# Kernel tuning notes

Hardware: AMD Instinct MI355X
Metric: run time of the kernel (lower is better)

The kernel has to match this reference:

```python
import jax, jax.numpy as jnp
import numpy as np

N_ENT, E, M, STEPS, B, H, C = 500000, 128, 8, 3, 4096, 256, 16

def setup_inputs() -> dict:
    key = jax.random.key(0)
    ks = jax.random.split(key, 13)
    s = 0.05
    return {
        "entity_ids": jax.random.randint(ks[0], (B, STEPS + 1), 0, N_ENT),
        "module_ids": jax.random.randint(ks[1], (B, STEPS), 0, M),
        "embedding": jax.random.normal(ks[2], (N_ENT, E), jnp.float32),
        "W_in": jax.random.normal(ks[3], (M, E, E), jnp.float32) * s,
        "b_in": jax.random.normal(ks[4], (M, E), jnp.float32) * s,
        "W_bias": jax.random.normal(ks[5], (M, E, E), jnp.float32) * s,
        "b_bias": jax.random.normal(ks[6], (M, E), jnp.float32) * s,
        "W_f": jax.random.normal(ks[7], (M, 2 * E, E), jnp.float32) * s,
        "b_f": jax.random.normal(ks[8], (M, E), jnp.float32) * s,
        "W1": jax.random.normal(ks[9], (E, H), jnp.float32) * s,
        "b1": jax.random.normal(ks[10], (H,), jnp.float32) * s,
        "W2": jax.random.normal(ks[11], (H, C), jnp.float32) * s,
        "b2": jax.random.normal(ks[12], (C,), jnp.float32) * s,
    }

def reference(entity_ids, module_ids, embedding, W_in, b_in, W_bias, b_bias,
              W_f, b_f, W1, b1, W2, b2):
    # x: [B, E] embedding of each path's start entity
    x = embedding[entity_ids[:, 0]]

    def step(x, inputs):
        mid, eid = inputs                      # [B], [B]
        bias = embedding[eid]                  # [B, E]
        h_in = jax.nn.relu(jnp.einsum('be,beo->bo', x, W_in[mid]) + b_in[mid])
        h_bi = jax.nn.relu(jnp.einsum('be,beo->bo', bias, W_bias[mid]) + b_bias[mid])
        h = jnp.concatenate([h_in, h_bi], axis=1)  # [B, 2E]
        x_new = jnp.tanh(jnp.einsum('bf,bfo->bo', h, W_f[mid]) + b_f[mid])
        return x_new, None

    xs = (module_ids.T, entity_ids[:, 1:].T)   # [STEPS, B] each
    x, _ = jax.lax.scan(step, x, xs)

    # classifier: Linear -> ReLU -> Linear
    h = jax.nn.relu(x @ W1 + b1)
    return h @ W2 + b2
```

## Files before the change

### kernel.cpp

```cpp
#include <hip/hip_runtime.h>

#define BB      4096
#define EE      128
#define MM      8
#define NSTEPS  3
#define HH      256
#define CC      16

#define TS      16
#define NBMAX   (BB/TS + MM)
#define FB      1024

#define NFRAGBLK 1096

#define ECONV0   1096
#define COUNT0   2120
#define GRID1    2168

typedef __attribute__((ext_vector_type(8))) short  bf16x8;
typedef __attribute__((ext_vector_type(4))) float  f32x4;

__device__ __forceinline__ unsigned short bf16_rn(float v) {
    unsigned u = __float_as_uint(v);
    return (unsigned short)((u + 0x7FFFu + ((u >> 16) & 1u)) >> 16);
}
__device__ __forceinline__ float bf16_f(unsigned short h) {
    return __uint_as_float(((unsigned)h) << 16);
}
__device__ __forceinline__ void split8(const float* v, bf16x8& hi, bf16x8& lo) {
    #pragma unroll
    for (int i = 0; i < 8; i++) {
        unsigned short h = bf16_rn(v[i]);
        hi[i] = (short)h;
        lo[i] = (short)bf16_rn(v[i] - bf16_f(h));
    }
}
__device__ __forceinline__ void split1(float v, unsigned short& h, unsigned short& l) {
    h = bf16_rn(v);
    l = bf16_rn(v - bf16_f(h));
}
#define MFMA(a,b,c) __builtin_amdgcn_mfma_f32_16x16x32_bf16((a),(b),(c),0,0,0)
__device__ __forceinline__ f32x4 mfma3(bf16x8 ah, bf16x8 al, bf16x8 bh, bf16x8 bl, f32x4 c) {
    c = MFMA(ah, bh, c);
    c = MFMA(ah, bl, c);
    c = MFMA(al, bh, c);
    return c;
}

__global__ __launch_bounds__(256) void convert_kernel(
    const int*   __restrict__ entity_ids, const int* __restrict__ module_ids,
    const float* __restrict__ embedding,
    const float* __restrict__ W_in, const float* __restrict__ W_bias,
    const float* __restrict__ W_f,  const float* __restrict__ W1,
    const float* __restrict__ W2,
    unsigned short* __restrict__ wf,
    unsigned short* __restrict__ x0h, unsigned short* __restrict__ x0l,
    unsigned short* __restrict__ ebh, unsigned short* __restrict__ ebl,
    int* __restrict__ wcnt)
{
    const int b = blockIdx.x, tid = threadIdx.x;
    if (b < NFRAGBLK) {
        unsigned short* dhi = wf + (size_t)b * FB;
        unsigned short* dlo = dhi + 512;
        #pragma unroll
        for (int half = 0; half < 2; half++) {
            const int el = tid + half * 256;
            const int ln = el >> 3, j = el & 7;
            const int krel = ((ln >> 4) << 3) + j;
            const int nrel = ln & 15;
            float v;
            if (b < 512) {
                const int bb = b & 255;
                const int kc = bb & 3, nt = (bb >> 2) & 7, m = bb >> 5;
                const float* src = (b < 256 ? W_in : W_bias) + (size_t)m * EE * EE;
                v = src[(size_t)(kc*32 + krel) * EE + nt*16 + nrel];
            } else if (b < 1024) {
                const int bb = b - 512;
                const int kc = bb & 7, nt = (bb >> 3) & 7, m = bb >> 6;
                v = W_f[(size_t)m * 2*EE*EE + (size_t)(kc*32 + krel) * EE + nt*16 + nrel];
            } else if (b < 1088) {
                const int bb = b - 1024;
                const int kc = bb & 3, nt = bb >> 2;
                v = W1[(size_t)(kc*32 + krel) * HH + nt*16 + nrel];
            } else {
                const int kc = b - 1088;
                v = W2[(size_t)(kc*32 + krel) * CC + nrel];
            }
            split1(v, dhi[el], dlo[el]);
        }
    } else if (b < COUNT0) {
        const int u = b - ECONV0;
        const int g = u >> 8, wb = u & 255;
        const int rloc = tid >> 4, cpart = tid & 15;
        const int s = wb*16 + rloc;
        const int eid = entity_ids[s*(NSTEPS+1) + g];
        const float* src = embedding + (size_t)eid*EE + cpart*8;
        float vv[8];
        *(float4*)(vv)     = *(const float4*)(src);
        *(float4*)(vv + 4) = *(const float4*)(src + 4);
        bf16x8 hi, lo;
        split8(vv, hi, lo);
        unsigned short* dh = (g == 0 ? x0h : ebh + (size_t)(g-1)*BB*EE) + (size_t)s*EE + cpart*8;
        unsigned short* dl = (g == 0 ? x0l : ebl + (size_t)(g-1)*BB*EE) + (size_t)s*EE + cpart*8;
        *(bf16x8*)dh = hi;
        *(bf16x8*)dl = lo;
    } else {
        const int u = b - COUNT0;
        const int t = u >> 4, chunk = u & 15;
        const int wave = tid >> 6, lane = tid & 63;
        const int s = chunk*256 + wave*64 + lane;
        const int m = module_ids[s*NSTEPS + t];
        unsigned long long bal[MM];
        #pragma unroll
        for (int k = 0; k < MM; k++) bal[k] = __ballot(m == k);
        if (lane < MM)
            wcnt[((t*16 + chunk)*4 + wave)*MM + lane] = __popcll(bal[lane]);
    }
}

__global__ __launch_bounds__(256) void plan_kernel(
    const int* __restrict__ wcnt,
    int* __restrict__ blockMod,
    int* __restrict__ gbase,
    int* __restrict__ perm)
{
    __shared__ int scnt[NSTEPS*16*4*MM];
    __shared__ int tot [NSTEPS][MM];
    __shared__ int base[NSTEPS][MM];
    const int tid = threadIdx.x;

    for (int i = tid; i < NSTEPS*16*4*MM; i += 256) scnt[i] = wcnt[i];
    for (int i = tid; i < NSTEPS*NBMAX*TS; i += 256) perm[i] = -1;
    __syncthreads();

    if (tid < NSTEPS*MM) {
        const int t = tid / MM, m = tid % MM;
        int s = 0;
        for (int sl = 0; sl < 64; sl++) s += scnt[(t*64 + sl)*MM + m];
        tot[t][m] = s;
    }
    __syncthreads();
    if (tid < NSTEPS) {
        const int t = tid;
        int blk = 0;
        for (int m = 0; m < MM; m++) {
            base[t][m] = blk * TS;
            const int nb = (tot[t][m] + TS - 1) / TS;
            for (int b = 0; b < nb; b++) blockMod[t*NBMAX + blk + b] = m;
            blk += nb;
        }
        for (; blk < NBMAX; blk++) blockMod[t*NBMAX + blk] = -1;
    }
    __syncthreads();
    if (tid < NSTEPS*MM) {
        const int t = tid / MM, m = tid % MM;
        int run = base[t][m];
        for (int sl = 0; sl < 64; sl++) {
            const int idx = (t*64 + sl)*MM + m;
            gbase[idx] = run;
            run += scnt[idx];
        }
    }
}

__global__ __launch_bounds__(256) void scatter_kernel(
    const int* __restrict__ module_ids,
    const int* __restrict__ gbase,
    int* __restrict__ perm)
{
    const int u = blockIdx.x;
    const int t = u >> 4, chunk = u & 15;
    const int tid = threadIdx.x, wave = tid >> 6, lane = tid & 63;
    __shared__ int gb[4*MM];
    if (tid < 4*MM) gb[tid] = gbase[((t*16 + chunk)*4)*MM + tid];
    __syncthreads();

    const int s = chunk*256 + wave*64 + lane;
    const int m = module_ids[s*NSTEPS + t];
    unsigned long long bal[MM];
    #pragma unroll
    for (int k = 0; k < MM; k++) bal[k] = __ballot(m == k);
    const unsigned long long below = (1ull << lane) - 1ull;
    const int rank = __popcll(bal[m] & below);
    perm[t*NBMAX*TS + gb[wave*MM + m] + rank] = s;
}

__global__ __launch_bounds__(512) void step_kernel(
    const int t,
    const unsigned short* __restrict__ x0h, const unsigned short* __restrict__ x0l,
    const unsigned short* __restrict__ ebh, const unsigned short* __restrict__ ebl,
    const float* __restrict__ b_in, const float* __restrict__ b_bias,
    const float* __restrict__ b_f,
    const unsigned short* __restrict__ wf,
    const int*   __restrict__ blockMod,
    const int*   __restrict__ perm,
    unsigned short* __restrict__ xsh, unsigned short* __restrict__ xsl)
{
    const int bid = blockIdx.x;
    const int m = blockMod[t*NBMAX + bid];
    if (m < 0) return;
    const int tid  = threadIdx.x;
    const int lane = tid & 63, wave = tid >> 6;
    const int row16 = lane & 15, quad = lane >> 4;
    const int pb = (t*NBMAX + bid)*TS;

    __shared__ __align__(16) unsigned short hfh[8][512];
    __shared__ __align__(16) unsigned short hfl[8][512];
    __shared__ int sids[TS];

    if (tid < TS) sids[tid] = perm[pb + tid];
    __syncthreads();

    const int sA  = sids[row16];
    const int sAc = sA < 0 ? 0 : sA;

    const unsigned short* xh_p = (t == 0 ? x0h : xsh) + (size_t)sAc*EE;
    const unsigned short* xl_p = (t == 0 ? x0l : xsl) + (size_t)sAc*EE;
    const unsigned short* eh_p = ebh + (size_t)t*BB*EE + (size_t)sAc*EE;
    const unsigned short* el_p = ebl + (size_t)t*BB*EE + (size_t)sAc*EE;

    bf16x8 xh[4], xl[4], eh[4], el_[4];
    #pragma unroll
    for (int kc = 0; kc < 4; kc++) {
        const int off = kc*32 + quad*8;
        xh[kc]  = *(const bf16x8*)(xh_p + off);
        xl[kc]  = *(const bf16x8*)(xl_p + off);
        eh[kc]  = *(const bf16x8*)(eh_p + off);
        el_[kc] = *(const bf16x8*)(el_p + off);
    }

    f32x4 aci = {0.f,0.f,0.f,0.f}, acb = {0.f,0.f,0.f,0.f};
    #pragma unroll
    for (int kc = 0; kc < 4; kc++) {
        const unsigned short* bI = wf + (size_t)((m*8 + wave)*4 + kc)*FB;
        const unsigned short* bB = wf + (size_t)(256 + (m*8 + wave)*4 + kc)*FB;
        const bf16x8 wih = *(const bf16x8*)(bI + lane*8);
        const bf16x8 wil = *(const bf16x8*)(bI + 512 + lane*8);
        const bf16x8 wbh = *(const bf16x8*)(bB + lane*8);
        const bf16x8 wbl = *(const bf16x8*)(bB + 512 + lane*8);
        aci = mfma3(xh[kc], xl[kc], wih, wil, aci);
        acb = mfma3(eh[kc], el_[kc], wbh, wbl, acb);
    }

    {
        const int col = wave*16 + row16;
        const float bin = b_in [m*EE + col];
        const float bbi = b_bias[m*EE + col];
        #pragma unroll
        for (int r = 0; r < 4; r++) {
            const int row = quad*4 + r;
            {
                const float v = fmaxf(aci[r] + bin, 0.f);
                const int k = col, kc = k >> 5;
                const int idx = (row + 16*((k >> 3) & 3))*8 + (k & 7);
                split1(v, hfh[kc][idx], hfl[kc][idx]);
            }
            {
                const float v = fmaxf(acb[r] + bbi, 0.f);
                const int k = EE + col, kc = k >> 5;
                const int idx = (row + 16*((k >> 3) & 3))*8 + (k & 7);
                split1(v, hfh[kc][idx], hfl[kc][idx]);
            }
        }
    }
    __syncthreads();

    f32x4 acf = {0.f,0.f,0.f,0.f};
    #pragma unroll
    for (int kc = 0; kc < 8; kc++) {
        const bf16x8 ah = *(const bf16x8*)(&hfh[kc][lane*8]);
        const bf16x8 al = *(const bf16x8*)(&hfl[kc][lane*8]);
        const unsigned short* bF = wf + (size_t)(512 + (m*8 + wave)*8 + kc)*FB;
        const bf16x8 wfh = *(const bf16x8*)(bF + lane*8);
        const bf16x8 wfl = *(const bf16x8*)(bF + 512 + lane*8);
        acf = mfma3(ah, al, wfh, wfl, acf);
    }
    {
        const int col = wave*16 + row16;
        const float bfv = b_f[m*EE + col];
        #pragma unroll
        for (int r = 0; r < 4; r++) {
            const int s = sids[quad*4 + r];
            if (s >= 0) {
                const float v = tanhf(acf[r] + bfv);
                unsigned short h, l;
                split1(v, h, l);
                xsh[(size_t)s*EE + col] = h;
                xsl[(size_t)s*EE + col] = l;
            }
        }
    }
}

__global__ __launch_bounds__(512) void final_kernel(
    const unsigned short* __restrict__ xsh, const unsigned short* __restrict__ xsl,
    const float* __restrict__ b1v, const float* __restrict__ b2,
    const unsigned short* __restrict__ wf,
    float* __restrict__ out)
{
    const int tid = threadIdx.x, bid = blockIdx.x;
    const int lane = tid & 63, wave = tid >> 6;
    const int row16 = lane & 15, quad = lane >> 4;
    const int sbase = bid * TS;

    __shared__ __align__(16) unsigned short hfh[8][512];
    __shared__ __align__(16) unsigned short hfl[8][512];
    __shared__ float red[8][TS][CC];

    const unsigned short* xh_p = xsh + (size_t)(sbase + row16)*EE;
    const unsigned short* xl_p = xsl + (size_t)(sbase + row16)*EE;
    bf16x8 xh[4], xl[4];
    #pragma unroll
    for (int kc = 0; kc < 4; kc++) {
        const int off = kc*32 + quad*8;
        xh[kc] = *(const bf16x8*)(xh_p + off);
        xl[kc] = *(const bf16x8*)(xl_p + off);
    }

    f32x4 a1[2] = {{0.f,0.f,0.f,0.f},{0.f,0.f,0.f,0.f}};
    #pragma unroll
    for (int i = 0; i < 2; i++) {
        const int nt = wave + 8*i;
        #pragma unroll
        for (int kc = 0; kc < 4; kc++) {
            const unsigned short* bW = wf + (size_t)(1024 + nt*4 + kc)*FB;
            const bf16x8 wh = *(const bf16x8*)(bW + lane*8);
            const bf16x8 wl = *(const bf16x8*)(bW + 512 + lane*8);
            a1[i] = mfma3(xh[kc], xl[kc], wh, wl, a1[i]);
        }
    }
    #pragma unroll
    for (int i = 0; i < 2; i++) {
        const int col = (wave + 8*i)*16 + row16;
        const float b = b1v[col];
        #pragma unroll
        for (int r = 0; r < 4; r++) {
            const int row = quad*4 + r;
            const float v = fmaxf(a1[i][r] + b, 0.f);
            const int kc = col >> 5;
            const int idx = (row + 16*((col >> 3) & 3))*8 + (col & 7);
            split1(v, hfh[kc][idx], hfl[kc][idx]);
        }
    }
    __syncthreads();

    f32x4 a2 = {0.f,0.f,0.f,0.f};
    {
        const int kc = wave;
        const bf16x8 ah = *(const bf16x8*)(&hfh[kc][lane*8]);
        const bf16x8 al = *(const bf16x8*)(&hfl[kc][lane*8]);
        const unsigned short* bW = wf + (size_t)(1088 + kc)*FB;
        const bf16x8 wh = *(const bf16x8*)(bW + lane*8);
        const bf16x8 wl = *(const bf16x8*)(bW + 512 + lane*8);
        a2 = mfma3(ah, al, wh, wl, a2);
    }
    #pragma unroll
    for (int r = 0; r < 4; r++) red[wave][quad*4 + r][row16] = a2[r];
    __syncthreads();

    if (tid < TS*CC) {
        const int s = tid >> 4, c = tid & 15;
        float v = b2[c];
        #pragma unroll
        for (int w = 0; w < 8; w++) v += red[w][s][c];
        out[(size_t)(sbase + s)*CC + c] = v;
    }
}

extern "C" void kernel_launch(void* const* d_in, const int* in_sizes, int n_in,
                              void* d_out, int out_size, void* d_ws, size_t ws_size,
                              hipStream_t stream) {
    const int*   entity_ids = (const int*)  d_in[0];
    const int*   module_ids = (const int*)  d_in[1];
    const float* embedding  = (const float*)d_in[2];
    const float* W_in   = (const float*)d_in[3];
    const float* b_in   = (const float*)d_in[4];
    const float* W_bias = (const float*)d_in[5];
    const float* b_bias = (const float*)d_in[6];
    const float* W_f    = (const float*)d_in[7];
    const float* b_f    = (const float*)d_in[8];
    const float* W1     = (const float*)d_in[9];
    const float* b1     = (const float*)d_in[10];
    const float* W2     = (const float*)d_in[11];
    const float* b2     = (const float*)d_in[12];
    float* out = (float*)d_out;

    char* ws = (char*)d_ws;
    int* blockMod = (int*)(ws + 0);
    int* perm     = (int*)(ws + 4096);
    int* wcnt     = (int*)(ws + 54784);
    int* gbase    = (int*)(ws + 60928);
    unsigned short* wfb = (unsigned short*)(ws + 131072);
    unsigned short* x0h = (unsigned short*)(ws + (4u<<20));
    unsigned short* x0l = (unsigned short*)(ws + (5u<<20));
    unsigned short* xsh = (unsigned short*)(ws + (6u<<20));
    unsigned short* xsl = (unsigned short*)(ws + (7u<<20));
    unsigned short* ebh = (unsigned short*)(ws + (8u<<20));
    unsigned short* ebl = (unsigned short*)(ws + (11u<<20));

    convert_kernel<<<GRID1, 256, 0, stream>>>(entity_ids, module_ids, embedding,
                                              W_in, W_bias, W_f, W1, W2,
                                              wfb, x0h, x0l, ebh, ebl, wcnt);
    plan_kernel<<<1, 256, 0, stream>>>(wcnt, blockMod, gbase, perm);
    scatter_kernel<<<48, 256, 0, stream>>>(module_ids, gbase, perm);
    for (int t = 0; t < NSTEPS; t++) {
        step_kernel<<<NBMAX, 512, 0, stream>>>(t, x0h, x0l, ebh, ebl,
                                               b_in, b_bias, b_f,
                                               wfb, blockMod, perm, xsh, xsl);
    }
    final_kernel<<<BB/TS, 512, 0, stream>>>(xsh, xsl, b1, b2, wfb, out);
}
```

Before: 370.1 us.

## Fuse all stages into one cooperative persistent kernel with grid syncs

Merges the convert, plan, scatter, three step kernels and the classifier into a single persistent mega kernel of 256 blocks. The kernel steps through phases separated by grid-wide cooperative syncs, and falls back to six separate launches if the cooperative launch fails. Module bucketing switches from a count/plan/scatter pipeline to per-wave ballots with atomicAdd into per-(step,module) counters, which removes the single-block plan kernel. The aim is to cut launch overhead and serial tiny kernels. In exchange, work is grid-strided over fewer blocks and every phase boundary costs a grid sync.

```diff
diff --git a/kernel.cpp b/kernel.cpp
--- a/kernel.cpp
+++ b/kernel.cpp
@@ -1,4 +1,7 @@
 #include <hip/hip_runtime.h>
+#include <hip/hip_cooperative_groups.h>
+
+namespace cg = cooperative_groups;
 
 #define BB      4096
 #define EE      128
@@ -8,14 +11,13 @@
 #define CC      16
 
 #define TS      16
-#define NBMAX   (BB/TS + MM)
 #define FB      1024
 
 #define NFRAGBLK 1096
 
-#define ECONV0   1096
-#define COUNT0   2120
-#define GRID1    2168
+#define CAP     4096
+#define GRIDN   256
+#define NV0     (NFRAGBLK + 512)
 
 typedef __attribute__((ext_vector_type(8))) short  bf16x8;
 typedef __attribute__((ext_vector_type(4))) float  f32x4;
@@ -47,323 +49,274 @@
     return c;
 }
 
-__global__ __launch_bounds__(256) void convert_kernel(
+__global__ __launch_bounds__(512, 2) void mega_kernel(
+    int ph_lo, int ph_hi, int coop,
     const int*   __restrict__ entity_ids, const int* __restrict__ module_ids,
     const float* __restrict__ embedding,
-    const float* __restrict__ W_in, const float* __restrict__ W_bias,
-    const float* __restrict__ W_f,  const float* __restrict__ W1,
-    const float* __restrict__ W2,
+    const float* __restrict__ W_in,  const float* __restrict__ b_in,
+    const float* __restrict__ W_bias,const float* __restrict__ b_bias,
+    const float* __restrict__ W_f,   const float* __restrict__ b_f,
+    const float* __restrict__ W1,    const float* __restrict__ b1v,
+    const float* __restrict__ W2,    const float* __restrict__ b2,
+    float* __restrict__ out,
+    int* __restrict__ cnt, int* __restrict__ perm,
     unsigned short* __restrict__ wf,
     unsigned short* __restrict__ x0h, unsigned short* __restrict__ x0l,
-    unsigned short* __restrict__ ebh, unsigned short* __restrict__ ebl,
-    int* __restrict__ wcnt)
+    unsigned short* __restrict__ xsh, unsigned short* __restrict__ xsl,
+    unsigned short* __restrict__ ebh, unsigned short* __restrict__ ebl)
 {
-    const int b = blockIdx.x, tid = threadIdx.x;
-    if (b < NFRAGBLK) {
-        unsigned short* dhi = wf + (size_t)b * FB;
-        unsigned short* dlo = dhi + 512;
-        #pragma unroll
-        for (int half = 0; half < 2; half++) {
-            const int el = tid + half * 256;
-            const int ln = el >> 3, j = el & 7;
-            const int krel = ((ln >> 4) << 3) + j;
-            const int nrel = ln & 15;
-            float v;
-            if (b < 512) {
-                const int bb = b & 255;
-                const int kc = bb & 3, nt = (bb >> 2) & 7, m = bb >> 5;
-                const float* src = (b < 256 ? W_in : W_bias) + (size_t)m * EE * EE;
-                v = src[(size_t)(kc*32 + krel) * EE + nt*16 + nrel];
-            } else if (b < 1024) {
-                const int bb = b - 512;
-                const int kc = bb & 7, nt = (bb >> 3) & 7, m = bb >> 6;
-                v = W_f[(size_t)m * 2*EE*EE + (size_t)(kc*32 + krel) * EE + nt*16 + nrel];
-            } else if (b < 1088) {
-                const int bb = b - 1024;
-                const int kc = bb & 3, nt = bb >> 2;
-                v = W1[(size_t)(kc*32 + krel) * HH + nt*16 + nrel];
-            } else {
-                const int kc = b - 1088;
-                v = W2[(size_t)(kc*32 + krel) * CC + nrel];
-            }
-            split1(v, dhi[el], dlo[el]);
-        }
-    } else if (b < COUNT0) {
-        const int u = b - ECONV0;
-        const int g = u >> 8, wb = u & 255;
-        const int rloc = tid >> 4, cpart = tid & 15;
-        const int s = wb*16 + rloc;
-        const int eid = entity_ids[s*(NSTEPS+1) + g];
-        const float* src = embedding + (size_t)eid*EE + cpart*8;
-        float vv[8];
-        *(float4*)(vv)     = *(const float4*)(src);
-        *(float4*)(vv + 4) = *(const float4*)(src + 4);
-        bf16x8 hi, lo;
-        split8(vv, hi, lo);
-        unsigned short* dh = (g == 0 ? x0h : ebh + (size_t)(g-1)*BB*EE) + (size_t)s*EE + cpart*8;
-        unsigned short* dl = (g == 0 ? x0l : ebl + (size_t)(g-1)*BB*EE) + (size_t)s*EE + cpart*8;
-        *(bf16x8*)dh = hi;
-        *(bf16x8*)dl = lo;
-    } else {
-        const int u = b - COUNT0;
-        const int t = u >> 4, chunk = u & 15;
-        const int wave = tid >> 6, lane = tid & 63;
-        const int s = chunk*256 + wave*64 + lane;
-        const int m = module_ids[s*NSTEPS + t];
-        unsigned long long bal[MM];
-        #pragma unroll
-        for (int k = 0; k < MM; k++) bal[k] = __ballot(m == k);
-        if (lane < MM)
-            wcnt[((t*16 + chunk)*4 + wave)*MM + lane] = __popcll(bal[lane]);
-    }
-}
-
-__global__ __launch_bounds__(256) void plan_kernel(
-    const int* __restrict__ wcnt,
-    int* __restrict__ blockMod,
-    int* __restrict__ gbase,
-    int* __restrict__ perm)
-{
-    __shared__ int scnt[NSTEPS*16*4*MM];
-    __shared__ int tot [NSTEPS][MM];
-    __shared__ int base[NSTEPS][MM];
-    const int tid = threadIdx.x;
-
-    for (int i = tid; i < NSTEPS*16*4*MM; i += 256) scnt[i] = wcnt[i];
-    for (int i = tid; i < NSTEPS*NBMAX*TS; i += 256) perm[i] = -1;
-    __syncthreads();
-
-    if (tid < NSTEPS*MM) {
-        const int t = tid / MM, m = tid % MM;
-        int s = 0;
-        for (int sl = 0; sl < 64; sl++) s += scnt[(t*64 + sl)*MM + m];
-        tot[t][m] = s;
-    }
-    __syncthreads();
-    if (tid < NSTEPS) {
-        const int t = tid;
-        int blk = 0;
-        for (int m = 0; m < MM; m++) {
-            base[t][m] = blk * TS;
-            const int nb = (tot[t][m] + TS - 1) / TS;
-            for (int b = 0; b < nb; b++) blockMod[t*NBMAX + blk + b] = m;
-            blk += nb;
-        }
-        for (; blk < NBMAX; blk++) blockMod[t*NBMAX + blk] = -1;
-    }
-    __syncthreads();
-    if (tid < NSTEPS*MM) {
-        const int t = tid / MM, m = tid % MM;
-        int run = base[t][m];
-        for (int sl = 0; sl < 64; sl++) {
-            const int idx = (t*64 + sl)*MM + m;
-            gbase[idx] = run;
-            run += scnt[idx];
-        }
-    }
-}
-
-__global__ __launch_bounds__(256) void scatter_kernel(
-    const int* __restrict__ module_ids,
-    const int* __restrict__ gbase,
-    int* __restrict__ perm)
-{
-    const int u = blockIdx.x;
-    const int t = u >> 4, chunk = u & 15;
-    const int tid = threadIdx.x, wave = tid >> 6, lane = tid & 63;
-    __shared__ int gb[4*MM];
-    if (tid < 4*MM) gb[tid] = gbase[((t*16 + chunk)*4)*MM + tid];
-    __syncthreads();
-
-    const int s = chunk*256 + wave*64 + lane;
-    const int m = module_ids[s*NSTEPS + t];
-    unsigned long long bal[MM];
-    #pragma unroll
-    for (int k = 0; k < MM; k++) bal[k] = __ballot(m == k);
-    const unsigned long long below = (1ull << lane) - 1ull;
-    const int rank = __popcll(bal[m] & below);
-    perm[t*NBMAX*TS + gb[wave*MM + m] + rank] = s;
-}
-
-__global__ __launch_bounds__(512) void step_kernel(
-    const int t,
-    const unsigned short* __restrict__ x0h, const unsigned short* __restrict__ x0l,
-    const unsigned short* __restrict__ ebh, const unsigned short* __restrict__ ebl,
-    const float* __restrict__ b_in, const float* __restrict__ b_bias,
-    const float* __restrict__ b_f,
-    const unsigned short* __restrict__ wf,
-    const int*   __restrict__ blockMod,
-    const int*   __restrict__ perm,
-    unsigned short* __restrict__ xsh, unsigned short* __restrict__ xsl)
-{
-    const int bid = blockIdx.x;
-    const int m = blockMod[t*NBMAX + bid];
-    if (m < 0) return;
     const int tid  = threadIdx.x;
+    const int bx   = blockIdx.x, gsz = gridDim.x;
     const int lane = tid & 63, wave = tid >> 6;
     const int row16 = lane & 15, quad = lane >> 4;
-    const int pb = (t*NBMAX + bid)*TS;
 
     __shared__ __align__(16) unsigned short hfh[8][512];
     __shared__ __align__(16) unsigned short hfl[8][512];
-    __shared__ int sids[TS];
-
-    if (tid < TS) sids[tid] = perm[pb + tid];
-    __syncthreads();
-
-    const int sA  = sids[row16];
-    const int sAc = sA < 0 ? 0 : sA;
-
-    const unsigned short* xh_p = (t == 0 ? x0h : xsh) + (size_t)sAc*EE;
-    const unsigned short* xl_p = (t == 0 ? x0l : xsl) + (size_t)sAc*EE;
-    const unsigned short* eh_p = ebh + (size_t)t*BB*EE + (size_t)sAc*EE;
-    const unsigned short* el_p = ebl + (size_t)t*BB*EE + (size_t)sAc*EE;
-
-    bf16x8 xh[4], xl[4], eh[4], el_[4];
-    #pragma unroll
-    for (int kc = 0; kc < 4; kc++) {
-        const int off = kc*32 + quad*8;
-        xh[kc]  = *(const bf16x8*)(xh_p + off);
-        xl[kc]  = *(const bf16x8*)(xl_p + off);
-        eh[kc]  = *(const bf16x8*)(eh_p + off);
-        el_[kc] = *(const bf16x8*)(el_p + off);
-    }
-
-    f32x4 aci = {0.f,0.f,0.f,0.f}, acb = {0.f,0.f,0.f,0.f};
-    #pragma unroll
-    for (int kc = 0; kc < 4; kc++) {
-        const unsigned short* bI = wf + (size_t)((m*8 + wave)*4 + kc)*FB;
-        const unsigned short* bB = wf + (size_t)(256 + (m*8 + wave)*4 + kc)*FB;
-        const bf16x8 wih = *(const bf16x8*)(bI + lane*8);
-        const bf16x8 wil = *(const bf16x8*)(bI + 512 + lane*8);
-        const bf16x8 wbh = *(const bf16x8*)(bB + lane*8);
-        const bf16x8 wbl = *(const bf16x8*)(bB + 512 + lane*8);
-        aci = mfma3(xh[kc], xl[kc], wih, wil, aci);
-        acb = mfma3(eh[kc], el_[kc], wbh, wbl, acb);
-    }
-
-    {
-        const int col = wave*16 + row16;
-        const float bin = b_in [m*EE + col];
-        const float bbi = b_bias[m*EE + col];
-        #pragma unroll
-        for (int r = 0; r < 4; r++) {
-            const int row = quad*4 + r;
-            {
-                const float v = fmaxf(aci[r] + bin, 0.f);
-                const int k = col, kc = k >> 5;
-                const int idx = (row + 16*((k >> 3) & 3))*8 + (k & 7);
-                split1(v, hfh[kc][idx], hfl[kc][idx]);
+    __shared__ int   sids[TS];
+    __shared__ float red[8][TS][CC];
+
+    cg::grid_group gg = cg::this_grid();
+
+    for (int ph = ph_lo; ph <= ph_hi; ph++) {
+        if (ph == 0) {
+            if (bx == 0 && tid < NSTEPS*MM) cnt[tid] = 0;
+            for (int vb = bx; vb < NV0; vb += gsz) {
+                if (vb < NFRAGBLK) {
+                    unsigned short* dhi = wf + (size_t)vb * FB;
+                    unsigned short* dlo = dhi + 512;
+                    const int el = tid;
+                    const int ln = el >> 3, j = el & 7;
+                    const int krel = ((ln >> 4) << 3) + j;
+                    const int nrel = ln & 15;
+                    float v;
+                    if (vb < 512) {
+                        const int bb = vb & 255;
+                        const int kc = bb & 3, nt = (bb >> 2) & 7, m = bb >> 5;
+                        const float* src = (vb < 256 ? W_in : W_bias) + (size_t)m * EE * EE;
+                        v = src[(size_t)(kc*32 + krel) * EE + nt*16 + nrel];
+                    } else if (vb < 1024) {
+                        const int bb = vb - 512;
+                        const int kc = bb & 7, nt = (bb >> 3) & 7, m = bb >> 6;
+                        v = W_f[(size_t)m * 2*EE*EE + (size_t)(kc*32 + krel) * EE + nt*16 + nrel];
+                    } else if (vb < 1088) {
+                        const int bb = vb - 1024;
+                        const int kc = bb & 3, nt = bb >> 2;
+                        v = W1[(size_t)(kc*32 + krel) * HH + nt*16 + nrel];
+                    } else {
+                        const int kc = vb - 1088;
+                        v = W2[(size_t)(kc*32 + krel) * CC + nrel];
+                    }
+                    split1(v, dhi[el], dlo[el]);
+                } else {
+                    const int u = vb - NFRAGBLK;
+                    const int rloc = tid >> 4, cpart = tid & 15;
+                    const int rglob = u*32 + rloc;
+                    const int g = rglob >> 12;
+                    const int s = rglob & (BB-1);
+                    const int eid = entity_ids[s*(NSTEPS+1) + g];
+                    const float* src = embedding + (size_t)eid*EE + cpart*8;
+                    float vv[8];
+                    *(float4*)(vv)     = *(const float4*)(src);
+                    *(float4*)(vv + 4) = *(const float4*)(src + 4);
+                    bf16x8 hi, lo;
+                    split8(vv, hi, lo);
+                    unsigned short* dh = (g == 0 ? x0h : ebh + (size_t)(g-1)*BB*EE) + (size_t)s*EE + cpart*8;
+                    unsigned short* dl = (g == 0 ? x0l : ebl + (size_t)(g-1)*BB*EE) + (size_t)s*EE + cpart*8;
+                    *(bf16x8*)dh = hi;
+                    *(bf16x8*)dl = lo;
+                }
             }
-            {
-                const float v = fmaxf(acb[r] + bbi, 0.f);
-                const int k = EE + col, kc = k >> 5;
-                const int idx = (row + 16*((k >> 3) & 3))*8 + (k & 7);
-                split1(v, hfh[kc][idx], hfl[kc][idx]);
+        } else if (ph == 1) {
+            for (int vb = bx; vb < (NSTEPS*BB)/512; vb += gsz) {
+                const int gid = vb*512 + tid;
+                const int t = gid >> 12, s = gid & (BB-1);
+                const int m = module_ids[s*NSTEPS + t];
+                unsigned long long mybal = 0ull, lanebal = 0ull;
+                #pragma unroll
+                for (int k = 0; k < MM; k++) {
+                    const unsigned long long bk = __ballot(m == k);
+                    if (m == k)    mybal   = bk;
+                    if (lane == k) lanebal = bk;
+                }
+                int base = 0;
+                if (lane < MM) base = atomicAdd(&cnt[t*MM + lane], __popcll(lanebal));
+                const int mybase = __shfl(base, m);
+                const unsigned long long below = (1ull << lane) - 1ull;
+                const int rank = __popcll(mybal & below);
+                perm[((t*MM + m) << 12) + mybase + rank] = s;
+            }
+        } else if (ph <= 4) {
+            const int t = ph - 2;
+            int creg[8];
+            #pragma unroll
+            for (int k = 0; k < MM; k++) creg[k] = cnt[t*MM + k];
+            int NB = 0;
+            #pragma unroll
+            for (int k = 0; k < MM; k++) NB += (creg[k] + TS - 1) >> 4;
+
+            for (int vb = bx; vb < NB; vb += gsz) {
+                int m = -1, pref = 0, cm = 0, acc = 0;
+                #pragma unroll
+                for (int k = 0; k < MM; k++) {
+                    const int nbk = (creg[k] + TS - 1) >> 4;
+                    if (m < 0 && vb < acc + nbk) { m = k; pref = acc; cm = creg[k]; }
+                    acc += nbk;
+                }
+                const int chunk = vb - pref;
+
+                __syncthreads();
+                if (tid < TS) {
+                    const int sl = chunk*TS + tid;
+                    sids[tid] = (sl < cm) ? perm[((t*MM + m) << 12) + sl] : -1;
+                }
+                __syncthreads();
+
+                const int sA  = sids[row16];
+                const int sAc = sA < 0 ? 0 : sA;
+
+                const unsigned short* xh_p = (t == 0 ? x0h : xsh) + (size_t)sAc*EE;
+                const unsigned short* xl_p = (t == 0 ? x0l : xsl) + (size_t)sAc*EE;
+                const unsigned short* eh_p = ebh + (size_t)t*BB*EE + (size_t)sAc*EE;
+                const unsigned short* el_p = ebl + (size_t)t*BB*EE + (size_t)sAc*EE;
+
+                bf16x8 xh[4], xl[4], eh[4], el_[4];
+                #pragma unroll
+                for (int kc = 0; kc < 4; kc++) {
+                    const int off = kc*32 + quad*8;
+                    xh[kc]  = *(const bf16x8*)(xh_p + off);
+                    xl[kc]  = *(const bf16x8*)(xl_p + off);
+                    eh[kc]  = *(const bf16x8*)(eh_p + off);
+                    el_[kc] = *(const bf16x8*)(el_p + off);
+                }
+
+                f32x4 aci = {0.f,0.f,0.f,0.f}, acb = {0.f,0.f,0.f,0.f};
+                #pragma unroll
+                for (int kc = 0; kc < 4; kc++) {
+                    const unsigned short* bI = wf + (size_t)((m*8 + wave)*4 + kc)*FB;
+                    const unsigned short* bBp = wf + (size_t)(256 + (m*8 + wave)*4 + kc)*FB;
+                    const bf16x8 wih = *(const bf16x8*)(bI + lane*8);
+                    const bf16x8 wil = *(const bf16x8*)(bI + 512 + lane*8);
+                    const bf16x8 wbh = *(const bf16x8*)(bBp + lane*8);
+                    const bf16x8 wbl = *(const bf16x8*)(bBp + 512 + lane*8);
+                    aci = mfma3(xh[kc], xl[kc], wih, wil, aci);
+                    acb = mfma3(eh[kc], el_[kc], wbh, wbl, acb);
+                }
+
+                {
+                    const int col = wave*16 + row16;
+                    const float bin = b_in [m*EE + col];
+                    const float bbi = b_bias[m*EE + col];
+                    #pragma unroll
+                    for (int r = 0; r < 4; r++) {
+                        const int row = quad*4 + r;
+                        {
+                            const float v = fmaxf(aci[r] + bin, 0.f);
+                            const int k = col, kc = k >> 5;
+                            const int idx = (row + 16*((k >> 3) & 3))*8 + (k & 7);
+                            split1(v, hfh[kc][idx], hfl[kc][idx]);
+                        }
+                        {
+                            const float v = fmaxf(acb[r] + bbi, 0.f);
+                            const int k = EE + col, kc = k >> 5;
+                            const int idx = (row + 16*((k >> 3) & 3))*8 + (k & 7);
+                            split1(v, hfh[kc][idx], hfl[kc][idx]);
+                        }
+                    }
+                }
+                __syncthreads();
+
+                f32x4 acf = {0.f,0.f,0.f,0.f};
+                #pragma unroll
+                for (int kc = 0; kc < 8; kc++) {
+                    const bf16x8 ah = *(const bf16x8*)(&hfh[kc][lane*8]);
+                    const bf16x8 al = *(const bf16x8*)(&hfl[kc][lane*8]);
+                    const unsigned short* bF = wf + (size_t)(512 + (m*8 + wave)*8 + kc)*FB;
+                    const bf16x8 wfh = *(const bf16x8*)(bF + lane*8);
+                    const bf16x8 wfl = *(const bf16x8*)(bF + 512 + lane*8);
+                    acf = mfma3(ah, al, wfh, wfl, acf);
+                }
+                {
+                    const int col = wave*16 + row16;
+                    const float bfv = b_f[m*EE + col];
+                    #pragma unroll
+                    for (int r = 0; r < 4; r++) {
+                        const int s = sids[quad*4 + r];
+                        if (s >= 0) {
+                            const float v = tanhf(acf[r] + bfv);
+                            unsigned short h, l;
+                            split1(v, h, l);
+                            xsh[(size_t)s*EE + col] = h;
+                            xsl[(size_t)s*EE + col] = l;
+                        }
+                    }
+                }
+            }
+        } else {
+            for (int vb = bx; vb < BB/TS; vb += gsz) {
+                const int sbase = vb * TS;
+                __syncthreads();
+
+                const unsigned short* xh_p = xsh + (size_t)(sbase + row16)*EE;
+                const unsigned short* xl_p = xsl + (size_t)(sbase + row16)*EE;
+                bf16x8 xh[4], xl[4];
+                #pragma unroll
+                for (int kc = 0; kc < 4; kc++) {
+                    const int off = kc*32 + quad*8;
+                    xh[kc] = *(const bf16x8*)(xh_p + off);
+                    xl[kc] = *(const bf16x8*)(xl_p + off);
+                }
+
+                f32x4 a1[2] = {{0.f,0.f,0.f,0.f},{0.f,0.f,0.f,0.f}};
+                #pragma unroll
+                for (int i = 0; i < 2; i++) {
+                    const int nt = wave + 8*i;
+                    #pragma unroll
+                    for (int kc = 0; kc < 4; kc++) {
+                        const unsigned short* bW = wf + (size_t)(1024 + nt*4 + kc)*FB;
+                        const bf16x8 wh = *(const bf16x8*)(bW + lane*8);
+                        const bf16x8 wl = *(const bf16x8*)(bW + 512 + lane*8);
+                        a1[i] = mfma3(xh[kc], xl[kc], wh, wl, a1[i]);
+                    }
+                }
+                #pragma unroll
+                for (int i = 0; i < 2; i++) {
+                    const int col = (wave + 8*i)*16 + row16;
+                    const float b = b1v[col];
+                    #pragma unroll
+                    for (int r = 0; r < 4; r++) {
+                        const int row = quad*4 + r;
+                        const float v = fmaxf(a1[i][r] + b, 0.f);
+                        const int kc = col >> 5;
+                        const int idx = (row + 16*((col >> 3) & 3))*8 + (col & 7);
+                        split1(v, hfh[kc][idx], hfl[kc][idx]);
+                    }
+                }
+                __syncthreads();
+
+                f32x4 a2 = {0.f,0.f,0.f,0.f};
+                {
+                    const int kc = wave;
+                    const bf16x8 ah = *(const bf16x8*)(&hfh[kc][lane*8]);
+                    const bf16x8 al = *(const bf16x8*)(&hfl[kc][lane*8]);
+                    const unsigned short* bW = wf + (size_t)(1088 + kc)*FB;
+                    const bf16x8 wh = *(const bf16x8*)(bW + lane*8);
+                    const bf16x8 wl = *(const bf16x8*)(bW + 512 + lane*8);
+                    a2 = mfma3(ah, al, wh, wl, a2);
+                }
+                #pragma unroll
+                for (int r = 0; r < 4; r++) red[wave][quad*4 + r][row16] = a2[r];
+                __syncthreads();
+
+                if (tid < TS*CC) {
+                    const int s = tid >> 4, c = tid & 15;
+                    float v = b2[c];
+                    #pragma unroll
+                    for (int w = 0; w < 8; w++) v += red[w][s][c];
+                    out[(size_t)(sbase + s)*CC + c] = v;
+                }
             }
         }
-    }
-    __syncthreads();
-
-    f32x4 acf = {0.f,0.f,0.f,0.f};
-    #pragma unroll
-    for (int kc = 0; kc < 8; kc++) {
-        const bf16x8 ah = *(const bf16x8*)(&hfh[kc][lane*8]);
-        const bf16x8 al = *(const bf16x8*)(&hfl[kc][lane*8]);
-        const unsigned short* bF = wf + (size_t)(512 + (m*8 + wave)*8 + kc)*FB;
-        const bf16x8 wfh = *(const bf16x8*)(bF + lane*8);
-        const bf16x8 wfl = *(const bf16x8*)(bF + 512 + lane*8);
-        acf = mfma3(ah, al, wfh, wfl, acf);
-    }
-    {
-        const int col = wave*16 + row16;
-        const float bfv = b_f[m*EE + col];
-        #pragma unroll
-        for (int r = 0; r < 4; r++) {
-            const int s = sids[quad*4 + r];
-            if (s >= 0) {
-                const float v = tanhf(acf[r] + bfv);
-                unsigned short h, l;
-                split1(v, h, l);
-                xsh[(size_t)s*EE + col] = h;
-                xsl[(size_t)s*EE + col] = l;
-            }
-        }
-    }
-}
-
-__global__ __launch_bounds__(512) void final_kernel(
-    const unsigned short* __restrict__ xsh, const unsigned short* __restrict__ xsl,
-    const float* __restrict__ b1v, const float* __restrict__ b2,
-    const unsigned short* __restrict__ wf,
-    float* __restrict__ out)
-{
-    const int tid = threadIdx.x, bid = blockIdx.x;
-    const int lane = tid & 63, wave = tid >> 6;
-    const int row16 = lane & 15, quad = lane >> 4;
-    const int sbase = bid * TS;
-
-    __shared__ __align__(16) unsigned short hfh[8][512];
-    __shared__ __align__(16) unsigned short hfl[8][512];
-    __shared__ float red[8][TS][CC];
-
-    const unsigned short* xh_p = xsh + (size_t)(sbase + row16)*EE;
-    const unsigned short* xl_p = xsl + (size_t)(sbase + row16)*EE;
-    bf16x8 xh[4], xl[4];
-    #pragma unroll
-    for (int kc = 0; kc < 4; kc++) {
-        const int off = kc*32 + quad*8;
-        xh[kc] = *(const bf16x8*)(xh_p + off);
-        xl[kc] = *(const bf16x8*)(xl_p + off);
-    }
-
-    f32x4 a1[2] = {{0.f,0.f,0.f,0.f},{0.f,0.f,0.f,0.f}};
-    #pragma unroll
-    for (int i = 0; i < 2; i++) {
-        const int nt = wave + 8*i;
-        #pragma unroll
-        for (int kc = 0; kc < 4; kc++) {
-            const unsigned short* bW = wf + (size_t)(1024 + nt*4 + kc)*FB;
-            const bf16x8 wh = *(const bf16x8*)(bW + lane*8);
-            const bf16x8 wl = *(const bf16x8*)(bW + 512 + lane*8);
-            a1[i] = mfma3(xh[kc], xl[kc], wh, wl, a1[i]);
-        }
-    }
-    #pragma unroll
-    for (int i = 0; i < 2; i++) {
-        const int col = (wave + 8*i)*16 + row16;
-        const float b = b1v[col];
-        #pragma unroll
-        for (int r = 0; r < 4; r++) {
-            const int row = quad*4 + r;
-            const float v = fmaxf(a1[i][r] + b, 0.f);
-            const int kc = col >> 5;
-            const int idx = (row + 16*((col >> 3) & 3))*8 + (col & 7);
-            split1(v, hfh[kc][idx], hfl[kc][idx]);
-        }
-    }
-    __syncthreads();
-
-    f32x4 a2 = {0.f,0.f,0.f,0.f};
-    {
-        const int kc = wave;
-        const bf16x8 ah = *(const bf16x8*)(&hfh[kc][lane*8]);
-        const bf16x8 al = *(const bf16x8*)(&hfl[kc][lane*8]);
-        const unsigned short* bW = wf + (size_t)(1088 + kc)*FB;
-        const bf16x8 wh = *(const bf16x8*)(bW + lane*8);
-        const bf16x8 wl = *(const bf16x8*)(bW + 512 + lane*8);
-        a2 = mfma3(ah, al, wh, wl, a2);
-    }
-    #pragma unroll
-    for (int r = 0; r < 4; r++) red[wave][quad*4 + r][row16] = a2[r];
-    __syncthreads();
-
-    if (tid < TS*CC) {
-        const int s = tid >> 4, c = tid & 15;
-        float v = b2[c];
-        #pragma unroll
-        for (int w = 0; w < 8; w++) v += red[w][s][c];
-        out[(size_t)(sbase + s)*CC + c] = v;
+        if (coop && ph < ph_hi) gg.sync();
     }
 }
 
@@ -386,11 +339,9 @@
     float* out = (float*)d_out;
 
     char* ws = (char*)d_ws;
-    int* blockMod = (int*)(ws + 0);
-    int* perm     = (int*)(ws + 4096);
-    int* wcnt     = (int*)(ws + 54784);
-    int* gbase    = (int*)(ws + 60928);
-    unsigned short* wfb = (unsigned short*)(ws + 131072);
+    int* cnt  = (int*)(ws + 0);
+    int* perm = (int*)(ws + 4096);
+    unsigned short* wfb = (unsigned short*)(ws + (1u<<20));
     unsigned short* x0h = (unsigned short*)(ws + (4u<<20));
     unsigned short* x0l = (unsigned short*)(ws + (5u<<20));
     unsigned short* xsh = (unsigned short*)(ws + (6u<<20));
@@ -398,15 +349,21 @@
     unsigned short* ebh = (unsigned short*)(ws + (8u<<20));
     unsigned short* ebl = (unsigned short*)(ws + (11u<<20));
 
-    convert_kernel<<<GRID1, 256, 0, stream>>>(entity_ids, module_ids, embedding,
-                                              W_in, W_bias, W_f, W1, W2,
-                                              wfb, x0h, x0l, ebh, ebl, wcnt);
-    plan_kernel<<<1, 256, 0, stream>>>(wcnt, blockMod, gbase, perm);
-    scatter_kernel<<<48, 256, 0, stream>>>(module_ids, gbase, perm);
-    for (int t = 0; t < NSTEPS; t++) {
-        step_kernel<<<NBMAX, 512, 0, stream>>>(t, x0h, x0l, ebh, ebl,
-                                               b_in, b_bias, b_f,
-                                               wfb, blockMod, perm, xsh, xsl);
+    int lo = 0, hi = 5, coop = 1;
+    void* args[] = { &lo, &hi, &coop,
+                     &entity_ids, &module_ids, &embedding,
+                     &W_in, &b_in, &W_bias, &b_bias, &W_f, &b_f,
+                     &W1, &b1, &W2, &b2, &out,
+                     &cnt, &perm, &wfb, &x0h, &x0l, &xsh, &xsl, &ebh, &ebl };
+    hipError_t e = hipLaunchCooperativeKernel(
+        reinterpret_cast<const void*>(mega_kernel),
+        dim3(GRIDN), dim3(512), args, 0u, stream);
+    if (e != hipSuccess) {
+        (void)hipGetLastError();
+        for (int ph = 0; ph < 6; ph++)
+            mega_kernel<<<GRIDN, 512, 0, stream>>>(ph, ph, 0,
+                entity_ids, module_ids, embedding,
+                W_in, b_in, W_bias, b_bias, W_f, b_f, W1, b1, W2, b2, out,
+                cnt, perm, wfb, x0h, x0l, xsh, xsl, ebh, ebl);
     }
-    final_kernel<<<BB/TS, 512, 0, stream>>>(xsh, xsl, b1, b2, wfb, out);
-}
+}
```

Result: slower. 525.7 us (+42.0%).
